# Optimization experiments

Measured on AMD Instinct MI355X. Metric: run time of the kernel, lower is better.

## Reference

```python
import jax, jax.numpy as jnp
import numpy as np
from jax import lax

B = 8192
DEPTH = 4096
SCALES = 3
FLT = 4  # db2 filter length

_DB2_DEC_LO = np.array([-0.12940952255092145, 0.22414386804185735, 0.836516303737469, 0.48296291314469025], dtype=np.float32)
_DB2_DEC_HI = np.array([-0.48296291314469025, 0.836516303737469, 0.22414386804185735, 0.12940952255092145], dtype=np.float32)


def _coeff_lens(depth, flen, scales):
    # mirrors pywt.dwt_coeff_len(n, flen, 'zero') = floor((n + flen - 1) / 2)
    lens = [depth]
    for _ in range(scales):
        lens.append((lens[-1] + flen - 1) // 2)
    lens = lens[1:]
    lens.append(lens[-1])
    return lens  # e.g. [2049, 1026, 514, 514]

WAVE_DEPTH = int(np.sum(_coeff_lens(DEPTH, FLT, SCALES)))  # 4103


def setup_inputs() -> dict:
    key = jax.random.key(0)
    ks = jax.random.split(key, 5)
    x = jax.random.normal(ks[0], (B, DEPTH), dtype=jnp.float32)
    diag_b = 1.0 + 0.1 * jax.random.normal(ks[1], (DEPTH,), dtype=jnp.float32)
    diag_g = 1.0 + 0.1 * jax.random.normal(ks[2], (WAVE_DEPTH,), dtype=jnp.float32)
    diag_s = 1.0 + 0.1 * jax.random.normal(ks[3], (DEPTH,), dtype=jnp.float32)
    dec_lo = jnp.asarray(_DB2_DEC_LO)
    dec_hi = jnp.asarray(_DB2_DEC_HI)
    rec_lo = dec_lo[::-1]
    rec_hi = dec_hi[::-1]
    perm_idx = jax.random.permutation(ks[4], WAVE_DEPTH).astype(jnp.int32)
    return {"x": x, "diag_b": diag_b, "diag_g": diag_g, "diag_s": diag_s,
            "dec_lo": dec_lo, "dec_hi": dec_hi, "rec_lo": rec_lo, "rec_hi": rec_hi,
            "perm_idx": perm_idx}


def _forward(x, diag_b, diag_g, diag_s, dec_lo, dec_hi, rec_lo, rec_hi, perm_idx):
    L = dec_lo.shape[0]
    lens = _coeff_lens(x.shape[-1], L, SCALES)
    # mul_b: diag(vec) matmul == elementwise column scale
    a = x * diag_b
    # multi-level analysis DWT with 'zero' padding: full convolution, keep odd indices
    w_dec = jnp.stack([dec_lo[::-1], dec_hi[::-1]])[:, None, :]  # [2,1,L] (flip: lax does corr)
    details = []
    for _ in range(SCALES):
        y = lax.conv_general_dilated(a[:, None, :], w_dec, (2,), [(L - 2, L - 1)],
                                     dimension_numbers=("NCH", "OIH", "NCH"))
        a, d = y[:, 0, :], y[:, 1, :]
        details.append(d)
    c = jnp.concatenate([a] + details[::-1], axis=-1)  # [B, WAVE_DEPTH], [cA_s, cD_s, ..., cD_1]
    # mul_p: permutation matmul == column gather
    c = c[:, perm_idx]
    # mul_g
    c = c * diag_g
    # coefficient slicing exactly as in the original forward (incl. its start-update rule)
    rev = lens[::-1]
    coeffs = []
    start = 0
    for s_i in range(SCALES + 1):
        stop = start + rev[s_i]
        coeffs.append(c[:, start:stop])
        start = lens[s_i]
    # multi-level reconstruction (idwt, zero mode): zero-upsample, full conv, trim L-2 per side
    a = coeffs[0]
    w_rec = jnp.stack([rec_lo[::-1], rec_hi[::-1]])[None, :, :]  # [1,2,L]
    for d in coeffs[1:]:
        if a.shape[-1] == d.shape[-1] + 1:  # pywt waverec odd-length trim
            a = a[:, :-1]
        xin = jnp.stack([a, d], axis=1)  # [B,2,la]
        a = lax.conv_general_dilated(xin, w_rec, (1,), [(1, 1)], lhs_dilation=(2,),
                                     dimension_numbers=("NCH", "OIH", "NCH"))[:, 0, :]
    # mul_s
    return a * diag_s


def reference(x, diag_b, diag_g, diag_s, dec_lo, dec_hi, rec_lo, rec_hi, perm_idx):
    return _forward(x, diag_b, diag_g, diag_s, dec_lo, dec_hi, rec_lo, rec_hi, perm_idx)
```

## Files before the change

### kernel.cpp

```cpp
#include <hip/hip_runtime.h>


#define NT 512

__device__ __forceinline__ float getz(const float* b, int t, int N) {
    return ((unsigned)t < (unsigned)N) ? b[t] : 0.0f;
}

__global__ __launch_bounds__(NT, 8) void wavelet_fused(
    const float* __restrict__ x,
    const float* __restrict__ diag_b,
    const float* __restrict__ diag_g,
    const float* __restrict__ diag_s,
    const float* __restrict__ dec_lo,
    const float* __restrict__ dec_hi,
    const float* __restrict__ rec_lo,
    const float* __restrict__ rec_hi,
    const int*   __restrict__ perm_idx,
    float* __restrict__ out)
{
    __shared__ __align__(16) float A[4104];
    __shared__ __align__(16) float C[4104];

    const int tid = threadIdx.x;
    const long row = blockIdx.x;

    const float lo0=dec_lo[0], lo1=dec_lo[1], lo2=dec_lo[2], lo3=dec_lo[3];
    const float hi0=dec_hi[0], hi1=dec_hi[1], hi2=dec_hi[2], hi3=dec_hi[3];
    const float rl0=rec_lo[0], rl1=rec_lo[1], rl2=rec_lo[2], rl3=rec_lo[3];
    const float rh0=rec_hi[0], rh1=rec_hi[1], rh2=rec_hi[2], rh3=rec_hi[3];

    {
        const float4* xr = (const float4*)(x + row * 4096);
        const float4* bb = (const float4*)diag_b;
        float4* A4 = (float4*)A;
        for (int i = tid; i < 1024; i += NT) {
            float4 v = xr[i], w = bb[i];
            v.x *= w.x; v.y *= w.y; v.z *= w.z; v.w *= w.w;
            A4[i] = v;
        }
    }
    __syncthreads();

    for (int n = tid; n < 2049; n += NT) {
        float A0 = getz(A, 2*n+1, 4096);
        float A1 = getz(A, 2*n,   4096);
        float A2 = getz(A, 2*n-1, 4096);
        float A3 = getz(A, 2*n-2, 4096);
        C[n]        = lo0*A0 + lo1*A1 + lo2*A2 + lo3*A3;
        C[2054 + n] = hi0*A0 + hi1*A1 + hi2*A2 + hi3*A3;
    }
    __syncthreads();

    for (int n = tid; n < 1026; n += NT) {
        float A0 = getz(C, 2*n+1, 2049);
        float A1 = getz(C, 2*n,   2049);
        float A2 = getz(C, 2*n-1, 2049);
        float A3 = getz(C, 2*n-2, 2049);
        A[n]        = lo0*A0 + lo1*A1 + lo2*A2 + lo3*A3;
        A[1026 + n] = hi0*A0 + hi1*A1 + hi2*A2 + hi3*A3;
    }
    __syncthreads();

    for (int n = tid; n < 514; n += NT) {
        float A0 = getz(A, 2*n+1, 1026);
        float A1 = getz(A, 2*n,   1026);
        float A2 = getz(A, 2*n-1, 1026);
        float A3 = getz(A, 2*n-2, 1026);
        C[n]       = lo0*A0 + lo1*A1 + lo2*A2 + lo3*A3;
        C[514 + n] = hi0*A0 + hi1*A1 + hi2*A2 + hi3*A3;
    }
    for (int j = tid; j < 1026; j += NT) {
        C[1028 + j] = A[1026 + j];
    }
    __syncthreads();

    for (int i = tid; i < 4103; i += NT) {
        A[i] = C[perm_idx[i]] * diag_g[i];
    }
    __syncthreads();

    {
        float2* C2 = (float2*)C;
        for (int p = tid; p < 513; p += NT) {
            float a0 = A[p],        a1 = A[p+1];
            float d0 = A[2049 + p], d1 = A[2050 + p];
            float2 w;
            w.x = rl2*a0 + rl0*a1 + rh2*d0 + rh0*d1;
            w.y = rl3*a0 + rl1*a1 + rh3*d0 + rh1*d1;
            C2[p] = w;
        }
    }
    __syncthreads();

    {
        float2* R2 = (float2*)(C + 1028);
        for (int p = tid; p < 1025; p += NT) {
            float a0 = C[p],        a1 = C[p+1];
            float d0 = A[1026 + p], d1 = A[1027 + p];
            float2 w;
            w.x = rl2*a0 + rl0*a1 + rh2*d0 + rh0*d1;
            w.y = rl3*a0 + rl1*a1 + rh3*d0 + rh1*d1;
            R2[p] = w;
        }
    }
    __syncthreads();

    {
        const float4* ss = (const float4*)diag_s;
        float4* outr = (float4*)(out + row * 4096);
        for (int q = tid; q < 1024; q += NT) {
            int h = 2 * q;
            float a0 = C[1028 + h], a1 = C[1029 + h], a2 = C[1030 + h];
            float d0 = A[514 + h],  d1 = A[515 + h],  d2 = A[516 + h];
            float4 s4 = ss[q];
            float4 o;
            o.x = (rl2*a0 + rl0*a1 + rh2*d0 + rh0*d1) * s4.x;
            o.y = (rl3*a0 + rl1*a1 + rh3*d0 + rh1*d1) * s4.y;
            o.z = (rl2*a1 + rl0*a2 + rh2*d1 + rh0*d2) * s4.z;
            o.w = (rl3*a1 + rl1*a2 + rh3*d1 + rh1*d2) * s4.w;
            outr[q] = o;
        }
    }
}

extern "C" void kernel_launch(void* const* d_in, const int* in_sizes, int n_in,
                              void* d_out, int out_size, void* d_ws, size_t ws_size,
                              hipStream_t stream) {
    const float* x       = (const float*)d_in[0];
    const float* diag_b  = (const float*)d_in[1];
    const float* diag_g  = (const float*)d_in[2];
    const float* diag_s  = (const float*)d_in[3];
    const float* dec_lo  = (const float*)d_in[4];
    const float* dec_hi  = (const float*)d_in[5];
    const float* rec_lo  = (const float*)d_in[6];
    const float* rec_hi  = (const float*)d_in[7];
    const int*   perm    = (const int*)d_in[8];
    float* out = (float*)d_out;

    const int B = in_sizes[0] / 4096;
    wavelet_fused<<<B, NT, 0, stream>>>(
        x, diag_b, diag_g, diag_s, dec_lo, dec_hi, rec_lo, rec_hi, perm, out);
}
```

Before: 261.4 us.

## Pad shared buffers with zero halos and vectorize LDS accesses across wavelet stages

```diff
diff --git a/kernel.cpp b/kernel.cpp
--- a/kernel.cpp
+++ b/kernel.cpp
@@ -2,10 +2,6 @@
 
 
 #define NT 512
-
-__device__ __forceinline__ float getz(const float* b, int t, int N) {
-    return ((unsigned)t < (unsigned)N) ? b[t] : 0.0f;
-}
 
 __global__ __launch_bounds__(NT, 8) void wavelet_fused(
     const float* __restrict__ x,
@@ -19,8 +15,10 @@
     const int*   __restrict__ perm_idx,
     float* __restrict__ out)
 {
-    __shared__ __align__(16) float A[4104];
-    __shared__ __align__(16) float C[4104];
+    __shared__ __align__(16) float rawA[4 + 4112];
+    __shared__ __align__(16) float rawC[4 + 4112];
+    float* const A = rawA + 4;
+    float* const C = rawC + 4;
 
     const int tid = threadIdx.x;
     const long row = blockIdx.x;
@@ -39,87 +37,109 @@
             v.x *= w.x; v.y *= w.y; v.z *= w.z; v.w *= w.w;
             A4[i] = v;
         }
+        if (tid < 4)  rawA[tid] = 0.0f;
+        if (tid < 8)  A[4096 + tid] = 0.0f;
+        if (tid < 4)  rawC[tid] = 0.0f;
+        if (tid < 11) C[2049 + tid] = 0.0f;
     }
     __syncthreads();
 
     for (int n = tid; n < 2049; n += NT) {
-        float A0 = getz(A, 2*n+1, 4096);
-        float A1 = getz(A, 2*n,   4096);
-        float A2 = getz(A, 2*n-1, 4096);
-        float A3 = getz(A, 2*n-2, 4096);
-        C[n]        = lo0*A0 + lo1*A1 + lo2*A2 + lo3*A3;
-        C[2054 + n] = hi0*A0 + hi1*A1 + hi2*A2 + hi3*A3;
+        float2 u0 = *(const float2*)(A + 2*n - 2);
+        float2 u1 = *(const float2*)(A + 2*n);
+        C[n]        = lo0*u1.y + lo1*u1.x + lo2*u0.y + lo3*u0.x;
+        C[2060 + n] = hi0*u1.y + hi1*u1.x + hi2*u0.y + hi3*u0.x;
     }
     __syncthreads();
 
+    if (tid < 6) A[1026 + tid] = 0.0f;
     for (int n = tid; n < 1026; n += NT) {
-        float A0 = getz(C, 2*n+1, 2049);
-        float A1 = getz(C, 2*n,   2049);
-        float A2 = getz(C, 2*n-1, 2049);
-        float A3 = getz(C, 2*n-2, 2049);
-        A[n]        = lo0*A0 + lo1*A1 + lo2*A2 + lo3*A3;
-        A[1026 + n] = hi0*A0 + hi1*A1 + hi2*A2 + hi3*A3;
+        float2 u0 = *(const float2*)(C + 2*n - 2);
+        float2 u1 = *(const float2*)(C + 2*n);
+        A[n]        = lo0*u1.y + lo1*u1.x + lo2*u0.y + lo3*u0.x;
+        A[1032 + n] = hi0*u1.y + hi1*u1.x + hi2*u0.y + hi3*u0.x;
     }
     __syncthreads();
 
     for (int n = tid; n < 514; n += NT) {
-        float A0 = getz(A, 2*n+1, 1026);
-        float A1 = getz(A, 2*n,   1026);
-        float A2 = getz(A, 2*n-1, 1026);
-        float A3 = getz(A, 2*n-2, 1026);
-        C[n]       = lo0*A0 + lo1*A1 + lo2*A2 + lo3*A3;
-        C[514 + n] = hi0*A0 + hi1*A1 + hi2*A2 + hi3*A3;
+        float2 u0 = *(const float2*)(A + 2*n - 2);
+        float2 u1 = *(const float2*)(A + 2*n);
+        C[n]       = lo0*u1.y + lo1*u1.x + lo2*u0.y + lo3*u0.x;
+        C[514 + n] = hi0*u1.y + hi1*u1.x + hi2*u0.y + hi3*u0.x;
     }
-    for (int j = tid; j < 1026; j += NT) {
-        C[1028 + j] = A[1026 + j];
+    for (int j = tid; j < 513; j += NT) {
+        *(float2*)(C + 1028 + 2*j) = *(const float2*)(A + 1032 + 2*j);
     }
     __syncthreads();
 
-    for (int i = tid; i < 4103; i += NT) {
-        A[i] = C[perm_idx[i]] * diag_g[i];
+    for (int q = tid; q < 1025; q += NT) {
+        int4  pj = ((const int4*)perm_idx)[q];
+        float4 g4 = ((const float4*)diag_g)[q];
+        float4 v;
+        v.x = C[pj.x + (pj.x >= 2054 ? 6 : 0)] * g4.x;
+        v.y = C[pj.y + (pj.y >= 2054 ? 6 : 0)] * g4.y;
+        v.z = C[pj.z + (pj.z >= 2054 ? 6 : 0)] * g4.z;
+        v.w = C[pj.w + (pj.w >= 2054 ? 6 : 0)] * g4.w;
+        ((float4*)A)[q] = v;
+    }
+    if (tid < 3) {
+        int i = 4100 + tid;
+        int j = perm_idx[i];
+        A[i] = C[j + (j >= 2054 ? 6 : 0)] * diag_g[i];
     }
     __syncthreads();
 
-    {
-        float2* C2 = (float2*)C;
-        for (int p = tid; p < 513; p += NT) {
-            float a0 = A[p],        a1 = A[p+1];
-            float d0 = A[2049 + p], d1 = A[2050 + p];
-            float2 w;
-            w.x = rl2*a0 + rl0*a1 + rh2*d0 + rh0*d1;
-            w.y = rl3*a0 + rl1*a1 + rh3*d0 + rh1*d1;
-            C2[p] = w;
-        }
+    for (int u = tid; u < 257; u += NT) {
+        int p0 = 2 * u;
+        float a0v = A[p0],        a1v = A[p0 + 1],    a2v = A[p0 + 2];
+        float d0v = A[2049 + p0], d1v = A[2050 + p0], d2v = A[2051 + p0];
+        float4 w;
+        w.x = rl2*a0v + rl0*a1v + rh2*d0v + rh0*d1v;
+        w.y = rl3*a0v + rl1*a1v + rh3*d0v + rh1*d1v;
+        w.z = rl2*a1v + rl0*a2v + rh2*d1v + rh0*d2v;
+        w.w = rl3*a1v + rl1*a2v + rh3*d1v + rh1*d2v;
+        if (u < 256) *(float4*)(C + 4*u) = w;
+        else         { C[4*u] = w.x; C[4*u + 1] = w.y; }
     }
     __syncthreads();
 
-    {
-        float2* R2 = (float2*)(C + 1028);
-        for (int p = tid; p < 1025; p += NT) {
-            float a0 = C[p],        a1 = C[p+1];
-            float d0 = A[1026 + p], d1 = A[1027 + p];
-            float2 w;
-            w.x = rl2*a0 + rl0*a1 + rh2*d0 + rh0*d1;
-            w.y = rl3*a0 + rl1*a1 + rh3*d0 + rh1*d1;
-            R2[p] = w;
-        }
+    for (int u = tid; u < 513; u += NT) {
+        int p0 = 2 * u;
+        float a0v = C[p0], a1v = C[p0 + 1], a2v = C[p0 + 2];
+        float2 dd = *(const float2*)(A + 1026 + p0);
+        float d2v = A[1028 + p0];
+        float4 w;
+        w.x = rl2*a0v + rl0*a1v + rh2*dd.x + rh0*dd.y;
+        w.y = rl3*a0v + rl1*a1v + rh3*dd.x + rh1*dd.y;
+        w.z = rl2*a1v + rl0*a2v + rh2*dd.y + rh0*d2v;
+        w.w = rl3*a1v + rl1*a2v + rh3*dd.y + rh1*d2v;
+        if (u < 512) *(float4*)(C + 1028 + 4*u) = w;
+        else         { C[1028 + 4*u] = w.x; C[1028 + 4*u + 1] = w.y; }
     }
     __syncthreads();
 
     {
         const float4* ss = (const float4*)diag_s;
         float4* outr = (float4*)(out + row * 4096);
-        for (int q = tid; q < 1024; q += NT) {
-            int h = 2 * q;
-            float a0 = C[1028 + h], a1 = C[1029 + h], a2 = C[1030 + h];
-            float d0 = A[514 + h],  d1 = A[515 + h],  d2 = A[516 + h];
-            float4 s4 = ss[q];
-            float4 o;
-            o.x = (rl2*a0 + rl0*a1 + rh2*d0 + rh0*d1) * s4.x;
-            o.y = (rl3*a0 + rl1*a1 + rh3*d0 + rh1*d1) * s4.y;
-            o.z = (rl2*a1 + rl0*a2 + rh2*d1 + rh0*d2) * s4.z;
-            o.w = (rl3*a1 + rl1*a2 + rh3*d1 + rh1*d2) * s4.w;
-            outr[q] = o;
+        for (int u = tid; u < 512; u += NT) {
+            int b = 1028 + 4 * u;
+            float4 aa = *(const float4*)(C + b);
+            float a4v = C[b + 4];
+            float2 dd0 = *(const float2*)(A + 514 + 4*u);
+            float2 dd1 = *(const float2*)(A + 516 + 4*u);
+            float d4v  = A[518 + 4*u];
+            float4 s0 = ss[2*u], s1 = ss[2*u + 1];
+            float4 o0, o1;
+            o0.x = (rl2*aa.x + rl0*aa.y + rh2*dd0.x + rh0*dd0.y) * s0.x;
+            o0.y = (rl3*aa.x + rl1*aa.y + rh3*dd0.x + rh1*dd0.y) * s0.y;
+            o0.z = (rl2*aa.y + rl0*aa.z + rh2*dd0.y + rh0*dd1.x) * s0.z;
+            o0.w = (rl3*aa.y + rl1*aa.z + rh3*dd0.y + rh1*dd1.x) * s0.w;
+            o1.x = (rl2*aa.z + rl0*aa.w + rh2*dd1.x + rh0*dd1.y) * s1.x;
+            o1.y = (rl3*aa.z + rl1*aa.w + rh3*dd1.x + rh1*dd1.y) * s1.y;
+            o1.z = (rl2*aa.w + rl0*a4v  + rh2*dd1.y + rh0*d4v ) * s1.z;
+            o1.w = (rl3*aa.w + rl1*a4v  + rh3*dd1.y + rh1*d4v ) * s1.w;
+            outr[2*u]     = o0;
+            outr[2*u + 1] = o1;
         }
     }
 }
```

New measurement: 257.0 us. About the same (-1.7%).
